# Kernel optimization log

Measured on AMD Instinct MI355X. Metric: run time of the kernel, lower is better.

The kernel has to match this reference:

```python
import jax, jax.numpy as jnp
import numpy as np

B, N, D = 4, 10000, 64
C, E = 2, 160000  # adj channels, edges per (graph, channel)
EPS = 1e-10


def setup_inputs() -> dict:
    key = jax.random.key(0)
    k1, k2, k3 = jax.random.split(key, 3)
    inputs = jax.random.normal(k1, (B, N, D), dtype=jnp.float32)
    edge_idx = jax.random.randint(k2, (B, C, E, 2), 0, N, dtype=jnp.int32)
    weight_a = 0.1 * jax.random.normal(k3, (C, 2 * D, 1), dtype=jnp.float32)
    return {"inputs": inputs, "edge_idx": edge_idx, "weight_a": weight_a}


def _gat_channel(x, idx, wa):
    # x: [N, D], idx: [E, 2] (col 0 = scatter/dst node, col 1 = gather/src node), wa: [2D, 1]
    n = x.shape[0]
    a1 = x[idx[:, 1]]                      # [E, D]
    a2 = x[idx[:, 0]]                      # [E, D]
    score = jnp.concatenate([a1, a2], axis=1) @ wa   # [E, 1]
    e = jnp.exp(jax.nn.leaky_relu(score, negative_slope=0.2))  # [E, 1]
    denom = jax.ops.segment_sum(e, idx[:, 0], num_segments=n)  # [N, 1]  (ii @ e)
    denom_e = denom[idx[:, 1]]             # [E, 1]  (faithful to original: gather by idx[:,1])
    alpha = e / (denom_e + EPS)            # [E, 1]
    r = jax.ops.segment_sum(alpha * a1, idx[:, 0], num_segments=n)  # [N, D]
    return jax.nn.sigmoid(r)


def _gat_graph(x, idx_all, weight_a):
    # x: [N, D], idx_all: [C, E, 2], weight_a: [C, 2D, 1]
    per_ch = jax.vmap(_gat_channel, in_axes=(None, 0, 0))(x, idx_all, weight_a)  # [C, N, D]
    return per_ch.sum(axis=0)


def reference(inputs, edge_idx, weight_a):
    # inputs: [B, N, D], edge_idx: [B, C, E, 2], weight_a: [C, 2D, 1]
    return jax.vmap(_gat_graph, in_axes=(0, 0, None))(inputs, edge_idx, weight_a)
```

## Files before the change

kernel.cpp:

```cpp
#include <hip/hip_runtime.h>

#define B_ 4
#define N_ 10000
#define D_ 64
#define C_ 2
#define E_ 160000
#define BC_ (B_ * C_)
#define SH2_ 7
#define NB2_ 128
#define G2_ 79
#define CAPF_ 2560
#define NBLK_ 125
#define EPT_ 5
#define EPB_ (256 * EPT_)
#define EPS_ 1e-10f

__global__ void gat_y(const float* __restrict__ x, const float* __restrict__ wa,
                      float* __restrict__ y1, float* __restrict__ y0) {
    int bc = blockIdx.x & 7;
    int n  = (blockIdx.x >> 3) * 256 + threadIdx.x;
    if (n >= N_) return;
    int b = bc / C_, c = bc % C_;
    const float4* xr = (const float4*)(x + ((size_t)b * N_ + n) * D_);
    const float4* w1 = (const float4*)(wa + (size_t)c * 2 * D_);
    const float4* w0 = w1 + D_ / 4;
    float a = 0.f, bb = 0.f;
#pragma unroll
    for (int i = 0; i < D_ / 4; ++i) {
        float4 xv = xr[i];
        float4 u = w1[i], v = w0[i];
        a  += xv.x * u.x + xv.y * u.y + xv.z * u.z + xv.w * u.w;
        bb += xv.x * v.x + xv.y * v.y + xv.z * v.z + xv.w * v.w;
    }
    y1[bc * N_ + n] = a;
    y0[bc * N_ + n] = bb;
}

__global__ void gat_bucket(const int* __restrict__ eidx, int* __restrict__ gcount,
                           unsigned int* __restrict__ bpack) {
    int bc  = blockIdx.x & 7;
    int blk = blockIdx.x >> 3;
    const int2* ep = (const int2*)eidx + (size_t)bc * E_ + (size_t)blk * EPB_;
    __shared__ int hist[G2_];
    __shared__ int cur[G2_];
    if (threadIdx.x < G2_) hist[threadIdx.x] = 0;
    __syncthreads();
    int2 ev[EPT_];
#pragma unroll
    for (int k = 0; k < EPT_; ++k) {
        ev[k] = ep[k * 256 + threadIdx.x];
        atomicAdd(&hist[ev[k].x >> SH2_], 1);
    }
    __syncthreads();
    if (threadIdx.x < G2_)
        cur[threadIdx.x] = atomicAdd(&gcount[bc * G2_ + threadIdx.x], hist[threadIdx.x]);
    __syncthreads();
#pragma unroll
    for (int k = 0; k < EPT_; ++k) {
        int g   = ev[k].x >> SH2_;
        int off = atomicAdd(&cur[g], 1);
        bpack[((size_t)bc * G2_ + g) * CAPF_ + off] =
            ((unsigned int)(ev[k].x & (NB2_ - 1)) << 16) | (unsigned int)ev[k].y;
    }
}

__global__ void gat_fine(const unsigned int* __restrict__ bpack,
                         const int* __restrict__ gcount,
                         const float* __restrict__ y1, const float* __restrict__ y0,
                         unsigned short* __restrict__ csr_i1, float* __restrict__ csr_ee,
                         int* __restrict__ rs_s, int* __restrict__ rs_e,
                         float* __restrict__ rd) {
    int bc = blockIdx.x & 7;
    int g  = blockIdx.x >> 3;
    int K  = gcount[bc * G2_ + g];
    int R  = (bc * G2_ + g) * CAPF_;
    const unsigned int* bp = bpack + R;
    const float* y1p = y1 + bc * N_;
    int tid = threadIdx.x;

    __shared__ int   cnt[NB2_], excl[NB2_], cur[NB2_], sd[NB2_];
    __shared__ float y0l[NB2_];
    __shared__ unsigned short li1[CAPF_];
    __shared__ float lee[CAPF_];

    int node = g * NB2_ + tid;
    if (tid < NB2_) {
        cnt[tid] = 0;
        y0l[tid] = (node < N_) ? y0[bc * N_ + node] : 0.f;
    }
    __syncthreads();

    for (int j = tid; j < K; j += 256)
        atomicAdd(&cnt[bp[j] >> 16], 1);
    __syncthreads();

    int v = 0;
    if (tid < NB2_) { v = cnt[tid]; sd[tid] = v; }
    __syncthreads();
    for (int off = 1; off < NB2_; off <<= 1) {
        int t = (tid < NB2_ && tid >= off) ? sd[tid - off] : 0;
        __syncthreads();
        if (tid < NB2_) sd[tid] += t;
        __syncthreads();
    }
    if (tid < NB2_) {
        int ex = sd[tid] - v;
        excl[tid] = ex;
        cur[tid]  = ex;
        if (node < N_) {
            rs_s[bc * N_ + node] = R + ex;
            rs_e[bc * N_ + node] = R + ex + v;
        }
    }
    __syncthreads();

    for (int j = tid; j < K; j += 256) {
        unsigned int p = bp[j];
        int ln = p >> 16;
        int i1 = p & 0xffff;
        int slot = atomicAdd(&cur[ln], 1);
        li1[slot] = (unsigned short)i1;
        float sc = y1p[i1] + y0l[ln];
        lee[slot] = __expf(sc > 0.f ? sc : 0.2f * sc);
    }
    __syncthreads();

    if (tid < NB2_ && node < N_) {
        int s = excl[tid], t = s + v;
        float sum = 0.f;
        for (int j = s; j < t; ++j) sum += lee[j];
        rd[bc * N_ + node] = 1.f / (sum + EPS_);
    }
    for (int j = tid; j < K; j += 256) {
        csr_i1[R + j] = li1[j];
        csr_ee[R + j] = lee[j];
    }
}

__global__ void gat_acc(const float* __restrict__ x, const int* __restrict__ rs_s,
                        const int* __restrict__ rs_e,
                        const unsigned short* __restrict__ csr_i1,
                        const float* __restrict__ csr_ee, const float* __restrict__ rd,
                        float* __restrict__ out) {
    int lane = threadIdx.x & 63;
    int w    = threadIdx.x >> 6;
    int b    = blockIdx.x & 3;
    int nn   = blockIdx.x >> 2;
    int n    = nn * 2 + (w >> 1);
    int c    = w & 1;
    int bc = b * C_ + c;
    const float* xb  = x + (size_t)b * N_ * D_ + lane;
    const float* rdp = rd + bc * N_;
    int s = rs_s[bc * N_ + n], t = rs_e[bc * N_ + n];
    float acc = 0.f;
    for (int base = s; base < t; base += 64) {
        int m = t - base; if (m > 64) m = 64;
        int a = 0; float wgt = 0.f;
        if (lane < m) {
            a   = csr_i1[base + lane];
            wgt = csr_ee[base + lane] * rdp[a];
        }
        int mp = (m + 7) & ~7;
        for (int j = 0; j < mp; j += 8) {
            int   a0 = __shfl(a, j),     a1 = __shfl(a, j + 1);
            int   a2 = __shfl(a, j + 2), a3 = __shfl(a, j + 3);
            int   a4 = __shfl(a, j + 4), a5 = __shfl(a, j + 5);
            int   a6 = __shfl(a, j + 6), a7 = __shfl(a, j + 7);
            float w0 = __shfl(wgt, j),     w1 = __shfl(wgt, j + 1);
            float w2 = __shfl(wgt, j + 2), w3 = __shfl(wgt, j + 3);
            float w4 = __shfl(wgt, j + 4), w5 = __shfl(wgt, j + 5);
            float w6 = __shfl(wgt, j + 6), w7 = __shfl(wgt, j + 7);
            float x0 = xb[a0 * D_], x1 = xb[a1 * D_];
            float x2 = xb[a2 * D_], x3 = xb[a3 * D_];
            float x4 = xb[a4 * D_], x5 = xb[a5 * D_];
            float x6 = xb[a6 * D_], x7 = xb[a7 * D_];
            acc += w0 * x0;
            acc += w1 * x1;
            acc += w2 * x2;
            acc += w3 * x3;
            acc += w4 * x4;
            acc += w5 * x5;
            acc += w6 * x6;
            acc += w7 * x7;
        }
    }
    float sg = 1.f / (1.f + __expf(-acc));
    __shared__ float sh[2][64];
    if (c == 1) sh[w >> 1][lane] = sg;
    __syncthreads();
    if (c == 0) out[((size_t)b * N_ + n) * D_ + lane] = sg + sh[w >> 1][lane];
}

extern "C" void kernel_launch(void* const* d_in, const int* in_sizes, int n_in,
                              void* d_out, int out_size, void* d_ws, size_t ws_size,
                              hipStream_t stream) {
    const float* x    = (const float*)d_in[0];
    const int*   eidx = (const int*)d_in[1];
    const float* wa   = (const float*)d_in[2];
    float* out = (float*)d_out;

    int*   gcount = (int*)d_ws;
    float* y1     = (float*)d_ws + 1024;
    float* y0     = y1 + BC_ * N_;
    float* rd     = y0 + BC_ * N_;
    int*   rs_s   = (int*)(rd + BC_ * N_);
    int*   rs_e   = rs_s + BC_ * N_;
    unsigned int* bpack  = (unsigned int*)(rs_e + BC_ * N_);
    float*        csr_ee = (float*)(bpack + (size_t)BC_ * G2_ * CAPF_);
    unsigned short* csr_i1 = (unsigned short*)(csr_ee + (size_t)BC_ * G2_ * CAPF_);

    hipMemsetAsync(gcount, 0, BC_ * G2_ * sizeof(int), stream);

    gat_y     <<<BC_ * 40,    256, 0, stream>>>(x, wa, y1, y0);
    gat_bucket<<<BC_ * NBLK_, 256, 0, stream>>>(eidx, gcount, bpack);
    gat_fine  <<<BC_ * G2_,   256, 0, stream>>>(bpack, gcount, y1, y0,
                                                csr_i1, csr_ee, rs_s, rs_e, rd);
    gat_acc   <<<B_ * N_ / 2, 256, 0, stream>>>(x, rs_s, rs_e, csr_i1, csr_ee, rd, out);
}
```

Before: 137.8 us.

## Merge y-projection and edge bucketing kernels; stage bucketed edges in LDS for coalesced writes

Fuses the per-node score projection and the edge bucketing into one launch by splitting the grid by block index, which removes one kernel launch and lets both stages overlap. The bucketing step now sorts each block's edges by bucket in shared memory, using a prefix scan over per-bucket counts, before writing them out. Each bucket's run therefore goes to global memory as a contiguous range instead of scattered per-edge stores. The cost is more shared memory, extra barriers and a scan inside the bucketing blocks.

```diff
diff --git a/kernel.cpp b/kernel.cpp
--- a/kernel.cpp
+++ b/kernel.cpp
@@ -13,54 +13,84 @@
 #define NBLK_ 125
 #define EPT_ 5
 #define EPB_ (256 * EPT_)
+#define YBLK_ (BC_ * 40)
 #define EPS_ 1e-10f
 
-__global__ void gat_y(const float* __restrict__ x, const float* __restrict__ wa,
-                      float* __restrict__ y1, float* __restrict__ y0) {
-    int bc = blockIdx.x & 7;
-    int n  = (blockIdx.x >> 3) * 256 + threadIdx.x;
-    if (n >= N_) return;
-    int b = bc / C_, c = bc % C_;
-    const float4* xr = (const float4*)(x + ((size_t)b * N_ + n) * D_);
-    const float4* w1 = (const float4*)(wa + (size_t)c * 2 * D_);
-    const float4* w0 = w1 + D_ / 4;
-    float a = 0.f, bb = 0.f;
-#pragma unroll
-    for (int i = 0; i < D_ / 4; ++i) {
-        float4 xv = xr[i];
-        float4 u = w1[i], v = w0[i];
-        a  += xv.x * u.x + xv.y * u.y + xv.z * u.z + xv.w * u.w;
-        bb += xv.x * v.x + xv.y * v.y + xv.z * v.z + xv.w * v.w;
-    }
-    y1[bc * N_ + n] = a;
-    y0[bc * N_ + n] = bb;
-}
-
-__global__ void gat_bucket(const int* __restrict__ eidx, int* __restrict__ gcount,
-                           unsigned int* __restrict__ bpack) {
-    int bc  = blockIdx.x & 7;
-    int blk = blockIdx.x >> 3;
+__global__ void gat_yb(const float* __restrict__ x, const float* __restrict__ wa,
+                       float* __restrict__ y1, float* __restrict__ y0,
+                       const int* __restrict__ eidx, int* __restrict__ gcount,
+                       unsigned int* __restrict__ bpack) {
+    int tid = threadIdx.x;
+    if (blockIdx.x < YBLK_) {
+        int bc = blockIdx.x & 7;
+        int n  = (blockIdx.x >> 3) * 256 + tid;
+        if (n >= N_) return;
+        int b = bc / C_, c = bc % C_;
+        const float4* xr = (const float4*)(x + ((size_t)b * N_ + n) * D_);
+        const float4* w1 = (const float4*)(wa + (size_t)c * 2 * D_);
+        const float4* w0 = w1 + D_ / 4;
+        float a = 0.f, bb = 0.f;
+#pragma unroll
+        for (int i = 0; i < D_ / 4; ++i) {
+            float4 xv = xr[i];
+            float4 u = w1[i], v = w0[i];
+            a  += xv.x * u.x + xv.y * u.y + xv.z * u.z + xv.w * u.w;
+            bb += xv.x * v.x + xv.y * v.y + xv.z * v.z + xv.w * v.w;
+        }
+        y1[bc * N_ + n] = a;
+        y0[bc * N_ + n] = bb;
+        return;
+    }
+    int bid = blockIdx.x - YBLK_;
+    int bc  = bid & 7;
+    int blk = bid >> 3;
     const int2* ep = (const int2*)eidx + (size_t)bc * E_ + (size_t)blk * EPB_;
-    __shared__ int hist[G2_];
-    __shared__ int cur[G2_];
-    if (threadIdx.x < G2_) hist[threadIdx.x] = 0;
-    __syncthreads();
-    int2 ev[EPT_];
+    __shared__ int sd[128];
+    __shared__ int excl[G2_], cur[G2_], gbase[G2_];
+    __shared__ unsigned int stage[EPB_];
+    if (tid < 128) sd[tid] = 0;
+    __syncthreads();
+    unsigned int pk[EPT_];
+    int gg[EPT_];
 #pragma unroll
     for (int k = 0; k < EPT_; ++k) {
-        ev[k] = ep[k * 256 + threadIdx.x];
-        atomicAdd(&hist[ev[k].x >> SH2_], 1);
-    }
-    __syncthreads();
-    if (threadIdx.x < G2_)
-        cur[threadIdx.x] = atomicAdd(&gcount[bc * G2_ + threadIdx.x], hist[threadIdx.x]);
+        int2 v = ep[k * 256 + tid];
+        int g  = v.x >> SH2_;
+        gg[k]  = g;
+        pk[k]  = ((unsigned int)g << 21) |
+                 ((unsigned int)(v.x & (NB2_ - 1)) << 14) |
+                 (unsigned int)v.y;
+        atomicAdd(&sd[g], 1);
+    }
+    __syncthreads();
+    int cnt = (tid < 128) ? sd[tid] : 0;
+    for (int off = 1; off < 128; off <<= 1) {
+        int t = (tid < 128 && tid >= off) ? sd[tid - off] : 0;
+        __syncthreads();
+        if (tid < 128) sd[tid] += t;
+        __syncthreads();
+    }
+    if (tid < G2_) {
+        int ex = sd[tid] - cnt;
+        excl[tid]  = ex;
+        cur[tid]   = ex;
+        gbase[tid] = atomicAdd(&gcount[bc * G2_ + tid], cnt);
+    }
     __syncthreads();
 #pragma unroll
     for (int k = 0; k < EPT_; ++k) {
-        int g   = ev[k].x >> SH2_;
-        int off = atomicAdd(&cur[g], 1);
-        bpack[((size_t)bc * G2_ + g) * CAPF_ + off] =
-            ((unsigned int)(ev[k].x & (NB2_ - 1)) << 16) | (unsigned int)ev[k].y;
+        int slot = atomicAdd(&cur[gg[k]], 1);
+        stage[slot] = pk[k];
+    }
+    __syncthreads();
+#pragma unroll
+    for (int k = 0; k < EPT_; ++k) {
+        int idx = k * 256 + tid;
+        unsigned int p = stage[idx];
+        int g     = p >> 21;
+        int local = idx - excl[g];
+        bpack[((size_t)bc * G2_ + g) * CAPF_ + gbase[g] + local] =
+            (((p >> 14) & 127u) << 16) | (p & 16383u);
     }
 }
 
@@ -211,9 +241,8 @@
 
     hipMemsetAsync(gcount, 0, BC_ * G2_ * sizeof(int), stream);
 
-    gat_y     <<<BC_ * 40,    256, 0, stream>>>(x, wa, y1, y0);
-    gat_bucket<<<BC_ * NBLK_, 256, 0, stream>>>(eidx, gcount, bpack);
-    gat_fine  <<<BC_ * G2_,   256, 0, stream>>>(bpack, gcount, y1, y0,
-                                                csr_i1, csr_ee, rs_s, rs_e, rd);
-    gat_acc   <<<B_ * N_ / 2, 256, 0, stream>>>(x, rs_s, rs_e, csr_i1, csr_ee, rd, out);
-}
+    gat_yb  <<<YBLK_ + BC_ * NBLK_, 256, 0, stream>>>(x, wa, y1, y0, eidx, gcount, bpack);
+    gat_fine<<<BC_ * G2_,           256, 0, stream>>>(bpack, gcount, y1, y0,
+                                                      csr_i1, csr_ee, rs_s, rs_e, rd);
+    gat_acc <<<B_ * N_ / 2,         256, 0, stream>>>(x, rs_s, rs_e, csr_i1, csr_ee, rd, out);
+}
```

Result: faster. 133.1 us (-3.4%).
